# Kernel optimization log

Hardware: AMD Instinct MI355X
Metric: run time of the kernel (lower is better)

Reference implementation:

```python
import jax, jax.numpy as jnp
import numpy as np

DMODEL = 1024
NHEAD = 16
HDIM = DMODEL // NHEAD
CTXLEN = 2048
BATCH = 2


def setup_inputs() -> dict:
    key = jax.random.key(0)
    k_x, k_qkv, k_pw, k_pb = jax.random.split(key, 4)
    x = jax.random.normal(k_x, (BATCH, CTXLEN, DMODEL), dtype=jnp.float32)
    # nn.Linear weights: stored as [out, in]; init scale ~ 1/sqrt(in)
    s = 1.0 / np.sqrt(DMODEL)
    w_qkv = jax.random.uniform(k_qkv, (3 * DMODEL, DMODEL), minval=-s, maxval=s, dtype=jnp.float32)
    w_proj = jax.random.uniform(k_pw, (DMODEL, DMODEL), minval=-s, maxval=s, dtype=jnp.float32)
    b_proj = jax.random.uniform(k_pb, (DMODEL,), minval=-s, maxval=s, dtype=jnp.float32)
    return {"x": x, "w_qkv": w_qkv, "w_proj": w_proj, "b_proj": b_proj}


def reference(x, w_qkv, w_proj, b_proj):
    b, t, c = x.shape
    qkv = jnp.einsum('btc,oc->bto', x, w_qkv)  # [b, t, 3c]
    q, k, v = jnp.split(qkv, 3, axis=-1)
    # [b, nhead, t, hdim]
    q = q.reshape(b, t, NHEAD, HDIM).transpose(0, 2, 1, 3)
    k = k.reshape(b, t, NHEAD, HDIM).transpose(0, 2, 1, 3)
    v = v.reshape(b, t, NHEAD, HDIM).transpose(0, 2, 1, 3)
    # NOTE: original code MULTIPLIES by sqrt(hdim) (not the usual divide)
    att = jnp.einsum('bhqd,bhkd->bhqk', q, k) * (HDIM ** 0.5)
    causal = jnp.tril(jnp.ones((t, t), dtype=bool))  # [t, t]
    att = jnp.where(causal[None, None], att, -jnp.inf)
    att = jax.nn.softmax(att, axis=-1)
    y = jnp.einsum('bhqk,bhkd->bhqd', att, v)
    y = y.transpose(0, 2, 1, 3).reshape(b, t, c)
    return jnp.einsum('btc,oc->bto', y, w_proj) + b_proj
```

## Files before the change

kernel.cpp:

```cpp
#include <hip/hip_runtime.h>
#include <hip/hip_bf16.h>

#define DMODEL 1024
#define NHEAD 16
#define HDIM 64
#define CTXLEN 2048
#define BATCH 2
#define M_TOTAL (BATCH * CTXLEN)

typedef unsigned short ushort_t;
typedef __attribute__((ext_vector_type(8))) _Float16 f16x8;
typedef __attribute__((ext_vector_type(8))) unsigned short u16x8;
typedef __attribute__((ext_vector_type(4))) float f32x4;
typedef __attribute__((ext_vector_type(4))) unsigned short u16x4;

__device__ __forceinline__ unsigned short f32_f16(float f) {
    return __builtin_bit_cast(unsigned short, (_Float16)f);
}
__device__ __forceinline__ float f16_f32(unsigned short h) {
    return (float)__builtin_bit_cast(_Float16, h);
}
__device__ __forceinline__ float fast_exp2(float x) {
    return __builtin_amdgcn_exp2f(x);
}
__device__ __forceinline__ f32x4 mfma16f(f16x8 a, f16x8 b, f32x4 c) {
    return __builtin_amdgcn_mfma_f32_16x16x32_f16(a, b, c, 0, 0, 0);
}
__device__ __forceinline__ void gload_lds16(const ushort_t* g, ushort_t* l) {
    __builtin_amdgcn_global_load_lds(
        (const __attribute__((address_space(1))) void*)g,
        (__attribute__((address_space(3))) void*)l, 16, 0, 0);
}
__device__ __forceinline__ int unit_off(int qt) {
    if (qt < 8)  return qt;
    if (qt < 16) return 8 + (qt - 8) * 2;
    if (qt < 24) return 24 + (qt - 16) * 3;
    return 48 + (qt - 24) * 4;
}

__global__ __launch_bounds__(256)
void conv_f32_f16(const float* __restrict__ src, ushort_t* __restrict__ dst, int n4) {
    for (int i = blockIdx.x * blockDim.x + threadIdx.x; i < n4;
         i += gridDim.x * blockDim.x) {
        const float4 v = reinterpret_cast<const float4*>(src)[i];
        u16x4 o;
        o[0] = f32_f16(v.x); o[1] = f32_f16(v.y);
        o[2] = f32_f16(v.z); o[3] = f32_f16(v.w);
        reinterpret_cast<u16x4*>(dst)[i] = o;
    }
}

template<bool QKV_EPI>
__global__ __launch_bounds__(256)
void gemm_f16_nt(const ushort_t* __restrict__ A, const ushort_t* __restrict__ B,
                 const float* __restrict__ bias, float* __restrict__ C,
                 ushort_t* __restrict__ qf, ushort_t* __restrict__ kf,
                 ushort_t* __restrict__ vb,
                 int M, int N, int K) {
    __shared__ ushort_t lds[2 * 4096];

    const int tid  = threadIdx.x;
    const int lane = tid & 63;
    const int wave = tid >> 6;
    const int lc   = lane & 15;
    const int lg   = lane >> 4;
    const int wr   = wave >> 1;
    const int wc   = wave & 1;
    const int row0 = blockIdx.y * 128;
    const int col0 = blockIdx.x * 128;

    const int c0 = tid, c1 = 256 + tid;
    const int r0 = c0 >> 2, l0 = (c0 & 3) ^ ((c0 >> 3) & 3);
    const int r1 = c1 >> 2, l1 = (c1 & 3) ^ ((c1 >> 3) & 3);
    const size_t gaoff0 = (size_t)(row0 + r0) * K + l0 * 8;
    const size_t gaoff1 = (size_t)(row0 + r1) * K + l1 * 8;
    const size_t gboff0 = (size_t)(col0 + r0) * K + l0 * 8;
    const size_t gboff1 = (size_t)(col0 + r1) * K + l1 * 8;
    const int ld0 = c0 * 8, ld1 = c1 * 8;

    int aoff[4], boff[4];
    #pragma unroll
    for (int m = 0; m < 4; ++m) {
        const int ra = wr * 64 + m * 16 + lc;
        aoff[m] = ra * 32 + ((lg ^ ((ra >> 1) & 3)) * 8);
        const int rb = wc * 64 + m * 16 + lc;
        boff[m] = rb * 32 + ((lg ^ ((rb >> 1) & 3)) * 8);
    }

    f32x4 acc[4][4];
    const f32x4 zero4 = {0.f, 0.f, 0.f, 0.f};
    #pragma unroll
    for (int m = 0; m < 4; ++m)
        #pragma unroll
        for (int n = 0; n < 4; ++n) acc[m][n] = zero4;

    const int NT = K >> 5;

    auto stage = [&](int kt) {
        const int ko = kt * 32;
        gload_lds16(A + gaoff0 + ko, &lds[ld0]);
        gload_lds16(A + gaoff1 + ko, &lds[ld1]);
        gload_lds16(B + gboff0 + ko, &lds[4096 + ld0]);
        gload_lds16(B + gboff1 + ko, &lds[4096 + ld1]);
    };

    stage(0);
    for (int kt = 0; kt < NT; ++kt) {
        __syncthreads();
        f16x8 fa[4], fb[4];
        #pragma unroll
        for (int m = 0; m < 4; ++m) {
            fa[m] = *reinterpret_cast<const f16x8*>(&lds[aoff[m]]);
            fb[m] = *reinterpret_cast<const f16x8*>(&lds[4096 + boff[m]]);
        }
        __syncthreads();
        if (kt + 1 < NT) stage(kt + 1);
        #pragma unroll
        for (int m = 0; m < 4; ++m)
            #pragma unroll
            for (int n = 0; n < 4; ++n)
                acc[m][n] = mfma16f(fa[m], fb[n], acc[m][n]);
    }

    if (!QKV_EPI) {
        #pragma unroll
        for (int m = 0; m < 4; ++m)
            #pragma unroll
            for (int i = 0; i < 4; ++i) {
                const int r = row0 + wr * 64 + m * 16 + lg * 4 + i;
                #pragma unroll
                for (int n = 0; n < 4; ++n) {
                    const int c = col0 + wc * 64 + n * 16 + lc;
                    C[(size_t)r * N + c] = acc[m][n][i] + bias[c];
                }
            }
    } else {
        #pragma unroll
        for (int m = 0; m < 4; ++m)
            #pragma unroll
            for (int i = 0; i < 4; ++i) {
                const int r = row0 + wr * 64 + m * 16 + lg * 4 + i;
                const int bb = r >> 11;
                const int t  = r & 2047;
                #pragma unroll
                for (int n = 0; n < 4; ++n) {
                    const int cg  = col0 + wc * 64 + n * 16 + lc;
                    const int sec = cg >> 10;
                    const int ch  = cg & 1023;
                    const int hh  = ch >> 6;
                    const int d   = ch & 63;
                    const size_t off = (((size_t)(bb * NHEAD + hh)) * CTXLEN + t) * HDIM + d;
                    const unsigned short hv = f32_f16(acc[m][n][i]);
                    if (sec == 0)      qf[off] = hv;
                    else if (sec == 1) kf[off] = hv;
                    else               vb[off] = hv;
                }
            }
    }
}

__global__ __launch_bounds__(256)
void transpose_v(const ushort_t* __restrict__ vb, ushort_t* __restrict__ vt) {
    __shared__ ushort_t T[64][66];
    const int tt = blockIdx.x;
    const int bh = blockIdx.y;
    const int tid = threadIdx.x;
    const int r  = tid >> 2;
    const int c0 = (tid & 3) * 16;

    const ushort_t* src = vb + ((size_t)bh * CTXLEN + tt * 64) * HDIM;
    #pragma unroll
    for (int half = 0; half < 2; ++half) {
        const u16x8 v = *reinterpret_cast<const u16x8*>(&src[(size_t)r * HDIM + c0 + half * 8]);
        #pragma unroll
        for (int j = 0; j < 8; ++j) T[r][c0 + half * 8 + j] = v[j];
    }
    __syncthreads();
    ushort_t* dst = vt + ((size_t)bh * HDIM + r) * CTXLEN + tt * 64 + c0;
    u16x8 o0, o1;
    #pragma unroll
    for (int j = 0; j < 8; ++j) { o0[j] = T[c0 + j][r]; o1[j] = T[c0 + 8 + j][r]; }
    *reinterpret_cast<u16x8*>(&dst[0]) = o0;
    *reinterpret_cast<u16x8*>(&dst[8]) = o1;
}

#define SCALE_LOG2 11.5415603271f

__global__ __launch_bounds__(256)
void attn_fwd7(const ushort_t* __restrict__ qf, const ushort_t* __restrict__ kf,
               const ushort_t* __restrict__ vt,
               ushort_t* __restrict__ py, float* __restrict__ pml) {
    __shared__ ushort_t KH[2][4096];
    __shared__ ushort_t VT[2][4096];
    __shared__ ushort_t Ps[4][16][64];

    const int id    = blockIdx.x;
    const int bh    = id & 31;
    const int u_off = id >> 5;
    int qt, u;
    if (u_off < 8)       { qt = u_off;                          u = 0; }
    else if (u_off < 24) { const int t = u_off - 8;  qt = 8  + (t >> 1); u = t & 1; }
    else if (u_off < 48) { const int t = u_off - 24; const int q3 = t / 3; qt = 16 + q3; u = t - q3 * 3; }
    else                 { const int t = u_off - 48; qt = 24 + (t >> 2); u = t & 3; }
    const int total = qt + 1;
    const int nu    = (qt >> 3) + 1;
    const int base  = total / nu, rem = total % nu;
    const int kb0   = u * base + (u < rem ? u : rem);
    const int len   = base + (u < rem ? 1 : 0);
    const int slot  = bh * 80 + u_off;

    const int tid  = threadIdx.x;
    const int wave = tid >> 6;
    const int lane = tid & 63;
    const int lc   = lane & 15;
    const int lg   = lane >> 4;

    const ushort_t* kfb = kf + (size_t)bh * CTXLEN * HDIM;
    const ushort_t* vtb = vt + (size_t)bh * HDIM * CTXLEN;

    const int cA = tid, cB = 256 + tid;
    const int rA = cA >> 3, sgA = (cA & 7) ^ (rA & 7);
    const int rB = cB >> 3, sgB = (cB & 7) ^ (rB & 7);

    auto stage = [&](int kb, int buf) {
        const size_t koff = (size_t)(kb * 64);
        gload_lds16(kfb + (koff + rA) * HDIM + sgA * 8, &KH[buf][cA * 8]);
        gload_lds16(kfb + (koff + rB) * HDIM + sgB * 8, &KH[buf][cB * 8]);
        gload_lds16(vtb + (size_t)rA * CTXLEN + kb * 64 + sgA * 8, &VT[buf][cA * 8]);
        gload_lds16(vtb + (size_t)rB * CTXLEN + kb * 64 + sgB * 8, &VT[buf][cB * 8]);
    };

    const size_t qrow = (size_t)bh * CTXLEN + qt * 64 + wave * 16 + lc;
    f16x8 qfr[2];
    #pragma unroll
    for (int ds = 0; ds < 2; ++ds)
        qfr[ds] = *reinterpret_cast<const f16x8*>(&qf[qrow * HDIM + ds * 32 + lg * 8]);

    const f32x4 zero4 = {0.f, 0.f, 0.f, 0.f};
    f32x4 yacc[4];
    #pragma unroll
    for (int t = 0; t < 4; ++t) yacc[t] = zero4;
    float m_i = -1e30f, l_i = 0.f;

    stage(kb0, 0);
    __syncthreads();

    int cur = 0;
    for (int s = 0; s < len; ++s) {
        const int kb = kb0 + s;
        if (s + 1 < len) stage(kb + 1, cur ^ 1);

        f16x8 kfr[4][2];
        #pragma unroll
        for (int tc = 0; tc < 4; ++tc) {
            const int rk = tc * 16 + lc;
            #pragma unroll
            for (int ds = 0; ds < 2; ++ds) {
                const int a = rk * 64 + (((ds * 4 + lg) ^ (rk & 7)) * 8);
                kfr[tc][ds] = *reinterpret_cast<const f16x8*>(&KH[cur][a]);
            }
        }
        f16x8 vf[4][2];
        #pragma unroll
        for (int t = 0; t < 4; ++t) {
            const int rv = t * 16 + lc;
            #pragma unroll
            for (int ks = 0; ks < 2; ++ks) {
                const int a = rv * 64 + (((ks * 4 + lg) ^ (rv & 7)) * 8);
                vf[t][ks] = *reinterpret_cast<const f16x8*>(&VT[cur][a]);
            }
        }

        f32x4 sacc[4];
        #pragma unroll
        for (int tc = 0; tc < 4; ++tc) sacc[tc] = zero4;
        __builtin_amdgcn_s_setprio(1);
        #pragma unroll
        for (int tc = 0; tc < 4; ++tc)
            #pragma unroll
            for (int ds = 0; ds < 2; ++ds)
                sacc[tc] = mfma16f(kfr[tc][ds], qfr[ds], sacc[tc]);
        __builtin_amdgcn_s_setprio(0);

        const bool diag = (kb == qt);
        const int q_loc = wave * 16 + lc;
        float p[4][4];
        #pragma unroll
        for (int tc = 0; tc < 4; ++tc)
            #pragma unroll
            for (int i = 0; i < 4; ++i) {
                float uu = sacc[tc][i] * SCALE_LOG2;
                if (diag && (tc * 16 + lg * 4 + i) > q_loc) uu = -1e30f;
                p[tc][i] = uu;
            }
        float mx = p[0][0];
        #pragma unroll
        for (int tc = 0; tc < 4; ++tc)
            #pragma unroll
            for (int i = 0; i < 4; ++i) mx = fmaxf(mx, p[tc][i]);
        mx = fmaxf(mx, __shfl_xor(mx, 16));
        mx = fmaxf(mx, __shfl_xor(mx, 32));
        const float mnew = fmaxf(m_i, mx);
        const float corr = fast_exp2(m_i - mnew);
        float psum = 0.f;
        #pragma unroll
        for (int tc = 0; tc < 4; ++tc)
            #pragma unroll
            for (int i = 0; i < 4; ++i) {
                const float e = fast_exp2(p[tc][i] - mnew);
                p[tc][i] = e;
                psum += e;
            }
        psum += __shfl_xor(psum, 16);
        psum += __shfl_xor(psum, 32);
        l_i = l_i * corr + psum;
        m_i = mnew;
        #pragma unroll
        for (int t = 0; t < 4; ++t) yacc[t] *= corr;

        #pragma unroll
        for (int tc = 0; tc < 4; ++tc) {
            const int eb = tc * 16 + lg * 4;
            const int se = ((((eb >> 3) ^ (lc & 7)) << 3) | (eb & 7));
            u16x4 pk;
            #pragma unroll
            for (int i = 0; i < 4; ++i) pk[i] = f32_f16(p[tc][i]);
            *reinterpret_cast<u16x4*>(&Ps[wave][lc][se]) = pk;
        }
        f16x8 pa[2];
        #pragma unroll
        for (int ks = 0; ks < 2; ++ks) {
            const int sl = ((ks * 4 + lg) ^ (lc & 7)) << 3;
            pa[ks] = *reinterpret_cast<const f16x8*>(&Ps[wave][lc][sl]);
        }
        __builtin_amdgcn_s_setprio(1);
        #pragma unroll
        for (int t = 0; t < 4; ++t)
            #pragma unroll
            for (int ks = 0; ks < 2; ++ks)
                yacc[t] = mfma16f(vf[t][ks], pa[ks], yacc[t]);
        __builtin_amdgcn_s_setprio(0);

        __syncthreads();
        cur ^= 1;
    }

    const int row = wave * 16 + lc;
    ushort_t* prow = py + ((size_t)slot * 64 + row) * 64;
    #pragma unroll
    for (int t = 0; t < 4; ++t) {
        u16x4 o;
        #pragma unroll
        for (int i = 0; i < 4; ++i) o[i] = f32_f16(yacc[t][i]);
        *reinterpret_cast<u16x4*>(&prow[t * 16 + lg * 4]) = o;
    }
    if (lg == 0) {
        pml[(size_t)slot * 128 + row]      = m_i;
        pml[(size_t)slot * 128 + 64 + row] = l_i;
    }
}

__global__ __launch_bounds__(256)
void merge_attn(const ushort_t* __restrict__ py, const float* __restrict__ pml,
                ushort_t* __restrict__ yb) {
    const int bid = blockIdx.x;
    const int bh  = bid >> 5;
    const int qt  = bid & 31;
    const int b   = bh >> 4;
    const int h   = bh & 15;
    const int tid = threadIdx.x;
    const int row = tid >> 2;
    const int d0  = (tid & 3) * 16;

    const int nu    = (qt >> 3) + 1;
    const int sbase = bh * 80 + unit_off(qt);

    float mu[4], lu[4];
    float M = -1e30f;
    #pragma unroll
    for (int u = 0; u < 4; ++u) {
        if (u < nu) {
            mu[u] = pml[(size_t)(sbase + u) * 128 + row];
            lu[u] = pml[(size_t)(sbase + u) * 128 + 64 + row];
            M = fmaxf(M, mu[u]);
        } else { mu[u] = -1e30f; lu[u] = 0.f; }
    }
    float w[4], ltot = 0.f;
    #pragma unroll
    for (int u = 0; u < 4; ++u) {
        w[u] = (u < nu) ? fast_exp2(mu[u] - M) : 0.f;
        ltot += w[u] * lu[u];
    }

    float y[16];
    #pragma unroll
    for (int j = 0; j < 16; ++j) y[j] = 0.f;
    #pragma unroll
    for (int u = 0; u < 4; ++u) {
        if (u < nu) {
            const ushort_t* pr = py + ((size_t)(sbase + u) * 64 + row) * 64 + d0;
            const u16x8 a = *reinterpret_cast<const u16x8*>(&pr[0]);
            const u16x8 c = *reinterpret_cast<const u16x8*>(&pr[8]);
            #pragma unroll
            for (int j = 0; j < 8; ++j) {
                y[j]     += w[u] * f16_f32(a[j]);
                y[8 + j] += w[u] * f16_f32(c[j]);
            }
        }
    }
    const float inv = 1.0f / ltot;
    ushort_t* dst = yb + (size_t)(b * CTXLEN + qt * 64 + row) * DMODEL + h * HDIM + d0;
    u16x8 o0, o1;
    #pragma unroll
    for (int j = 0; j < 8; ++j) {
        o0[j] = f32_f16(y[j] * inv);
        o1[j] = f32_f16(y[8 + j] * inv);
    }
    *reinterpret_cast<u16x8*>(&dst[0]) = o0;
    *reinterpret_cast<u16x8*>(&dst[8]) = o1;
}

extern "C" void kernel_launch(void* const* d_in, const int* in_sizes, int n_in,
                              void* d_out, int out_size, void* d_ws, size_t ws_size,
                              hipStream_t stream) {
    const float* x      = (const float*)d_in[0];
    const float* w_qkv  = (const float*)d_in[1];
    const float* w_proj = (const float*)d_in[2];
    const float* b_proj = (const float*)d_in[3];
    float* out = (float*)d_out;

    char* ws = (char*)d_ws;
    ushort_t* wqf = (ushort_t*)(ws);
    ushort_t* wpf = (ushort_t*)(ws + 6291456);
    ushort_t* xf  = (ushort_t*)(ws + 8388608);
    ushort_t* qf  = (ushort_t*)(ws + 16777216);
    ushort_t* kf  = (ushort_t*)(ws + 25165824);
    ushort_t* vb  = (ushort_t*)(ws + 33554432);
    ushort_t* vt  = (ushort_t*)(ws + 41943040);
    ushort_t* py  = (ushort_t*)(ws + 50331648);
    float*    pml = (float*)   (ws + 71303168);
    ushort_t* yb  = xf;

    const dim3 blk(256);

    conv_f32_f16<<<dim3(2048), blk, 0, stream>>>(x, xf, M_TOTAL * DMODEL / 4);
    conv_f32_f16<<<dim3(2048), blk, 0, stream>>>(w_qkv, wqf, 3 * DMODEL * DMODEL / 4);
    conv_f32_f16<<<dim3(1024), blk, 0, stream>>>(w_proj, wpf, DMODEL * DMODEL / 4);

    gemm_f16_nt<true><<<dim3(3 * DMODEL / 128, M_TOTAL / 128), blk, 0, stream>>>(
        xf, wqf, nullptr, nullptr, qf, kf, vb, M_TOTAL, 3 * DMODEL, DMODEL);

    transpose_v<<<dim3(CTXLEN / 64, BATCH * NHEAD), blk, 0, stream>>>(vb, vt);

    attn_fwd7<<<dim3(2560), blk, 0, stream>>>(qf, kf, vt, py, pml);
    merge_attn<<<dim3(1024), blk, 0, stream>>>(py, pml, yb);

    gemm_f16_nt<false><<<dim3(DMODEL / 128, M_TOTAL / 128), blk, 0, stream>>>(
        yb, wpf, b_proj, out, nullptr, nullptr, nullptr, M_TOTAL, DMODEL, DMODEL);
}
```

Before: 126.9 us.

## Software-pipeline QK^T with softmax/PV, add lazy rescale, fuse conversion kernels

The attention loop is restructured so the QK^T MFMAs for block s overlap the softmax and PV of block s-1, with V fragments loaded one step ahead. The online softmax skips the max update and accumulator rescale when the new block max stays within 8 (log2 units) of the running max across the wave. The three fp32-to-fp16 conversion launches become one fused kernel. The cost is higher register pressure from the extra live accumulators and fragments, plus the risk of fp16 overflow in P when the max is allowed to drift.

Result: slower. 133.5 us (+5.2%).

```diff
diff --git a/kernel.cpp b/kernel.cpp
--- a/kernel.cpp
+++ b/kernel.cpp
@@ -39,14 +39,21 @@
 }
 
 __global__ __launch_bounds__(256)
-void conv_f32_f16(const float* __restrict__ src, ushort_t* __restrict__ dst, int n4) {
-    for (int i = blockIdx.x * blockDim.x + threadIdx.x; i < n4;
+void conv3_f32_f16(const float* __restrict__ a, ushort_t* __restrict__ da, int na4,
+                   const float* __restrict__ b, ushort_t* __restrict__ db, int nb4,
+                   const float* __restrict__ c, ushort_t* __restrict__ dc, int nc4) {
+    const int n = na4 + nb4 + nc4;
+    for (int i = blockIdx.x * blockDim.x + threadIdx.x; i < n;
          i += gridDim.x * blockDim.x) {
-        const float4 v = reinterpret_cast<const float4*>(src)[i];
+        const float* s; ushort_t* d; int j = i;
+        if (j < na4) { s = a; d = da; }
+        else if (j - na4 < nb4) { j -= na4; s = b; d = db; }
+        else { j -= na4 + nb4; s = c; d = dc; }
+        const float4 v = reinterpret_cast<const float4*>(s)[j];
         u16x4 o;
         o[0] = f32_f16(v.x); o[1] = f32_f16(v.y);
         o[2] = f32_f16(v.z); o[3] = f32_f16(v.w);
-        reinterpret_cast<u16x4*>(dst)[i] = o;
+        reinterpret_cast<u16x4*>(d)[j] = o;
     }
 }
 
@@ -187,7 +194,7 @@
 #define SCALE_LOG2 11.5415603271f
 
 __global__ __launch_bounds__(256)
-void attn_fwd7(const ushort_t* __restrict__ qf, const ushort_t* __restrict__ kf,
+void attn_fwd9(const ushort_t* __restrict__ qf, const ushort_t* __restrict__ kf,
                const ushort_t* __restrict__ vt,
                ushort_t* __restrict__ py, float* __restrict__ pml) {
     __shared__ ushort_t KH[2][4096];
@@ -242,54 +249,18 @@
     for (int t = 0; t < 4; ++t) yacc[t] = zero4;
     float m_i = -1e30f, l_i = 0.f;
 
-    stage(kb0, 0);
-    __syncthreads();
-
-    int cur = 0;
-    for (int s = 0; s < len; ++s) {
-        const int kb = kb0 + s;
-        if (s + 1 < len) stage(kb + 1, cur ^ 1);
-
-        f16x8 kfr[4][2];
-        #pragma unroll
-        for (int tc = 0; tc < 4; ++tc) {
-            const int rk = tc * 16 + lc;
-            #pragma unroll
-            for (int ds = 0; ds < 2; ++ds) {
-                const int a = rk * 64 + (((ds * 4 + lg) ^ (rk & 7)) * 8);
-                kfr[tc][ds] = *reinterpret_cast<const f16x8*>(&KH[cur][a]);
-            }
-        }
-        f16x8 vf[4][2];
-        #pragma unroll
-        for (int t = 0; t < 4; ++t) {
-            const int rv = t * 16 + lc;
-            #pragma unroll
-            for (int ks = 0; ks < 2; ++ks) {
-                const int a = rv * 64 + (((ks * 4 + lg) ^ (rv & 7)) * 8);
-                vf[t][ks] = *reinterpret_cast<const f16x8*>(&VT[cur][a]);
-            }
-        }
-
-        f32x4 sacc[4];
-        #pragma unroll
-        for (int tc = 0; tc < 4; ++tc) sacc[tc] = zero4;
-        __builtin_amdgcn_s_setprio(1);
-        #pragma unroll
-        for (int tc = 0; tc < 4; ++tc)
-            #pragma unroll
-            for (int ds = 0; ds < 2; ++ds)
-                sacc[tc] = mfma16f(kfr[tc][ds], qfr[ds], sacc[tc]);
-        __builtin_amdgcn_s_setprio(0);
-
-        const bool diag = (kb == qt);
+    f32x4 sacc_c[4];
+    f16x8 vfp[4][2];
+
+    auto softmax_pv = [&](int kb_c) {
+        const bool diag = (kb_c == qt);
         const int q_loc = wave * 16 + lc;
         float p[4][4];
         #pragma unroll
         for (int tc = 0; tc < 4; ++tc)
             #pragma unroll
             for (int i = 0; i < 4; ++i) {
-                float uu = sacc[tc][i] * SCALE_LOG2;
+                float uu = sacc_c[tc][i] * SCALE_LOG2;
                 if (diag && (tc * 16 + lg * 4 + i) > q_loc) uu = -1e30f;
                 p[tc][i] = uu;
             }
@@ -300,24 +271,38 @@
             for (int i = 0; i < 4; ++i) mx = fmaxf(mx, p[tc][i]);
         mx = fmaxf(mx, __shfl_xor(mx, 16));
         mx = fmaxf(mx, __shfl_xor(mx, 32));
-        const float mnew = fmaxf(m_i, mx);
-        const float corr = fast_exp2(m_i - mnew);
-        float psum = 0.f;
-        #pragma unroll
-        for (int tc = 0; tc < 4; ++tc)
-            #pragma unroll
-            for (int i = 0; i < 4; ++i) {
-                const float e = fast_exp2(p[tc][i] - mnew);
-                p[tc][i] = e;
-                psum += e;
-            }
-        psum += __shfl_xor(psum, 16);
-        psum += __shfl_xor(psum, 32);
-        l_i = l_i * corr + psum;
-        m_i = mnew;
-        #pragma unroll
-        for (int t = 0; t < 4; ++t) yacc[t] *= corr;
-
+        if (__all(mx <= m_i + 8.0f)) {
+            float psum = 0.f;
+            #pragma unroll
+            for (int tc = 0; tc < 4; ++tc)
+                #pragma unroll
+                for (int i = 0; i < 4; ++i) {
+                    const float e = fast_exp2(p[tc][i] - m_i);
+                    p[tc][i] = e;
+                    psum += e;
+                }
+            psum += __shfl_xor(psum, 16);
+            psum += __shfl_xor(psum, 32);
+            l_i += psum;
+        } else {
+            const float mnew = fmaxf(m_i, mx);
+            const float corr = fast_exp2(m_i - mnew);
+            float psum = 0.f;
+            #pragma unroll
+            for (int tc = 0; tc < 4; ++tc)
+                #pragma unroll
+                for (int i = 0; i < 4; ++i) {
+                    const float e = fast_exp2(p[tc][i] - mnew);
+                    p[tc][i] = e;
+                    psum += e;
+                }
+            psum += __shfl_xor(psum, 16);
+            psum += __shfl_xor(psum, 32);
+            l_i = l_i * corr + psum;
+            m_i = mnew;
+            #pragma unroll
+            for (int t = 0; t < 4; ++t) yacc[t] *= corr;
+        }
         #pragma unroll
         for (int tc = 0; tc < 4; ++tc) {
             const int eb = tc * 16 + lg * 4;
@@ -338,12 +323,89 @@
         for (int t = 0; t < 4; ++t)
             #pragma unroll
             for (int ks = 0; ks < 2; ++ks)
-                yacc[t] = mfma16f(vf[t][ks], pa[ks], yacc[t]);
+                yacc[t] = mfma16f(vfp[t][ks], pa[ks], yacc[t]);
         __builtin_amdgcn_s_setprio(0);
-
+    };
+
+    stage(kb0, 0);
+    __syncthreads();
+    if (len > 1) stage(kb0 + 1, 1);
+
+    {
+        f16x8 kfr[4][2];
+        #pragma unroll
+        for (int tc = 0; tc < 4; ++tc) {
+            const int rk = tc * 16 + lc;
+            #pragma unroll
+            for (int ds = 0; ds < 2; ++ds) {
+                const int a = rk * 64 + (((ds * 4 + lg) ^ (rk & 7)) * 8);
+                kfr[tc][ds] = *reinterpret_cast<const f16x8*>(&KH[0][a]);
+            }
+        }
+        #pragma unroll
+        for (int tc = 0; tc < 4; ++tc) sacc_c[tc] = zero4;
+        __builtin_amdgcn_s_setprio(1);
+        #pragma unroll
+        for (int tc = 0; tc < 4; ++tc)
+            #pragma unroll
+            for (int ds = 0; ds < 2; ++ds)
+                sacc_c[tc] = mfma16f(kfr[tc][ds], qfr[ds], sacc_c[tc]);
+        __builtin_amdgcn_s_setprio(0);
+        #pragma unroll
+        for (int t = 0; t < 4; ++t) {
+            const int rv = t * 16 + lc;
+            #pragma unroll
+            for (int ks = 0; ks < 2; ++ks) {
+                const int a = rv * 64 + (((ks * 4 + lg) ^ (rv & 7)) * 8);
+                vfp[t][ks] = *reinterpret_cast<const f16x8*>(&VT[0][a]);
+            }
+        }
+    }
+
+    for (int s = 1; s < len; ++s) {
         __syncthreads();
-        cur ^= 1;
-    }
+        if (s + 1 < len) stage(kb0 + s + 1, (s + 1) & 1);
+        const int bufs = s & 1;
+
+        f32x4 sacc_n[4];
+        {
+            f16x8 kfr[4][2];
+            #pragma unroll
+            for (int tc = 0; tc < 4; ++tc) {
+                const int rk = tc * 16 + lc;
+                #pragma unroll
+                for (int ds = 0; ds < 2; ++ds) {
+                    const int a = rk * 64 + (((ds * 4 + lg) ^ (rk & 7)) * 8);
+                    kfr[tc][ds] = *reinterpret_cast<const f16x8*>(&KH[bufs][a]);
+                }
+            }
+            #pragma unroll
+            for (int tc = 0; tc < 4; ++tc) sacc_n[tc] = zero4;
+            __builtin_amdgcn_s_setprio(1);
+            #pragma unroll
+            for (int tc = 0; tc < 4; ++tc)
+                #pragma unroll
+                for (int ds = 0; ds < 2; ++ds)
+                    sacc_n[tc] = mfma16f(kfr[tc][ds], qfr[ds], sacc_n[tc]);
+            __builtin_amdgcn_s_setprio(0);
+        }
+
+        softmax_pv(kb0 + s - 1);
+
+        #pragma unroll
+        for (int t = 0; t < 4; ++t) {
+            const int rv = t * 16 + lc;
+            #pragma unroll
+            for (int ks = 0; ks < 2; ++ks) {
+                const int a = rv * 64 + (((ks * 4 + lg) ^ (rv & 7)) * 8);
+                vfp[t][ks] = *reinterpret_cast<const f16x8*>(&VT[bufs][a]);
+            }
+        }
+        #pragma unroll
+        for (int tc = 0; tc < 4; ++tc) sacc_c[tc] = sacc_n[tc];
+    }
+
+    softmax_pv(kb0 + len - 1);
 
     const int row = wave * 16 + lc;
     ushort_t* prow = py + ((size_t)slot * 64 + row) * 64;
@@ -443,16 +505,17 @@
 
     const dim3 blk(256);
 
-    conv_f32_f16<<<dim3(2048), blk, 0, stream>>>(x, xf, M_TOTAL * DMODEL / 4);
-    conv_f32_f16<<<dim3(2048), blk, 0, stream>>>(w_qkv, wqf, 3 * DMODEL * DMODEL / 4);
-    conv_f32_f16<<<dim3(1024), blk, 0, stream>>>(w_proj, wpf, DMODEL * DMODEL / 4);
+    conv3_f32_f16<<<dim3(2048), blk, 0, stream>>>(
+        x, xf, M_TOTAL * DMODEL / 4,
+        w_qkv, wqf, 3 * DMODEL * DMODEL / 4,
+        w_proj, wpf, DMODEL * DMODEL / 4);
 
     gemm_f16_nt<true><<<dim3(3 * DMODEL / 128, M_TOTAL / 128), blk, 0, stream>>>(
         xf, wqf, nullptr, nullptr, qf, kf, vb, M_TOTAL, 3 * DMODEL, DMODEL);
 
     transpose_v<<<dim3(CTXLEN / 64, BATCH * NHEAD), blk, 0, stream>>>(vb, vt);
 
-    attn_fwd7<<<dim3(2560), blk, 0, stream>>>(qf, kf, vt, py, pml);
+    attn_fwd9<<<dim3(2560), blk, 0, stream>>>(qf, kf, vt, py, pml);
     merge_attn<<<dim3(1024), blk, 0, stream>>>(py, pml, yb);
 
     gemm_f16_nt<false><<<dim3(DMODEL / 128, M_TOTAL / 128), blk, 0, stream>>>(
```
